# Performance work log

Hardware: AMD Instinct MI355X
Metric: run time of the kernel (lower is better)

## Reference

```python
import jax, jax.numpy as jnp
import numpy as np

N_NODES = 100000
N_EDGES = 1600000
D_FEAT = 64
EPS = 1e-07


def setup_inputs() -> dict:
    key = jax.random.key(0)
    k_x, k_r, k_c, k_b = jax.random.split(key, 4)
    x = jax.random.normal(k_x, (N_NODES, D_FEAT), dtype=jnp.float32)
    row = jax.random.randint(k_r, (N_EDGES,), 0, N_NODES, dtype=jnp.int64)
    col = jax.random.randint(k_c, (N_EDGES,), 0, N_NODES, dtype=jnp.int64)
    beta = jax.random.uniform(k_b, (), dtype=jnp.float32)  # nn.Parameter ~ U(0,1)
    return {"x": x, "row": row, "col": col, "beta": beta}


def segment_softmax(logits, seg_ids, num_segments):
    # numerically stable softmax over edges grouped by seg_ids
    seg_max = jax.ops.segment_max(logits, seg_ids, num_segments=num_segments)
    e = jnp.exp(logits - seg_max[seg_ids])
    seg_sum = jax.ops.segment_sum(e, seg_ids, num_segments=num_segments)
    return e / seg_sum[seg_ids]


def reference(x, row, col, beta):
    A = x[row]                       # [E, d] gather at source of softmax group
    B = x[col]                       # [E, d]
    inner = jnp.sum(A * B, axis=1)   # [E]
    denom = jnp.linalg.norm(A, axis=1) * jnp.linalg.norm(B, axis=1) + EPS
    sim = beta * (inner / denom)     # [E]
    P = segment_softmax(sim, row, N_NODES)          # softmax grouped by row
    src = A * P[:, None]                            # [E, d]
    out = jax.ops.segment_sum(src, col, num_segments=N_NODES)  # scatter-add by col
    return out
```

## Files before the change

### kernel.cpp

```cpp
#include <hip/hip_runtime.h>
#include <math.h>

#define N_NODES 100000
#define N_EDGES 1600000
#define D_FEAT 64
#define EPS 1e-7f
#define NPART 8
#define COLS_PER_PART (N_NODES / NPART)
#define CAP 48
#define QSCALE 12000.0f
#define QINV (1.0f / 12000.0f)

typedef _Float16 h2 __attribute__((ext_vector_type(2)));

__device__ __forceinline__ unsigned pack2h(float a, float b) {
    h2 h;
    h.x = (_Float16)a;
    h.y = (_Float16)b;
    return __builtin_bit_cast(unsigned, h);
}

__device__ __forceinline__ float dot2acc(unsigned a, unsigned b, float c) {
#if __has_builtin(__builtin_amdgcn_fdot2)
    return __builtin_amdgcn_fdot2(__builtin_bit_cast(h2, a),
                                  __builtin_bit_cast(h2, b), c, false);
#else
    h2 ha = __builtin_bit_cast(h2, a), hb = __builtin_bit_cast(h2, b);
    return c + (float)ha.x * (float)hb.x + (float)ha.y * (float)hb.y;
#endif
}

__device__ __forceinline__ void fma2h(unsigned ab, float p, float& x, float& y) {
    h2 h = __builtin_bit_cast(h2, ab);
    x += p * (float)h.x;
    y += p * (float)h.y;
}

__device__ __forceinline__ float fastrcp(float x) {
#if __has_builtin(__builtin_amdgcn_rcpf)
    return __builtin_amdgcn_rcpf(x);
#else
    return 1.0f / x;
#endif
}

__global__ void prep_kernel(const float4* __restrict__ x4, uint2* __restrict__ xh2,
                            float* __restrict__ nrm) {
    int tid = blockIdx.x * blockDim.x + threadIdx.x;
    int node = tid >> 4;
    int lane = tid & 15;
    if (node >= N_NODES) return;
    float4 v = x4[(size_t)node * 16 + lane];
    uint2 h;
    h.x = pack2h(v.x, v.y);
    h.y = pack2h(v.z, v.w);
    xh2[(size_t)node * 16 + lane] = h;
    float s = v.x * v.x + v.y * v.y + v.z * v.z + v.w * v.w;
    s += __shfl_xor(s, 1);
    s += __shfl_xor(s, 2);
    s += __shfl_xor(s, 4);
    s += __shfl_xor(s, 8);
    if (lane == 0) nrm[node] = rsqrtf(s);
}

__global__ void place_kernel(const int* __restrict__ row, const int* __restrict__ col,
                             unsigned* __restrict__ cursor, unsigned* __restrict__ pay) {
    int part = blockIdx.x & (NPART - 1);
    int blk  = blockIdx.x >> 3;
    int nblk = gridDim.x >> 3;
    int lo = part * COLS_PER_PART;
    int hi = lo + COLS_PER_PART;
    int stride = nblk * blockDim.x;
    const int4* col4 = (const int4*)col;
    for (int e4 = blk * blockDim.x + threadIdx.x; e4 < (N_EDGES >> 2); e4 += stride) {
        int4 c = col4[e4];
        int e = e4 << 2;
        if (c.x >= lo && c.x < hi) {
            unsigned pos = atomicAdd(&cursor[c.x], 1u);
            if (pos < CAP) pay[(size_t)c.x * CAP + pos] = (unsigned)row[e] << 15;
        }
        if (c.y >= lo && c.y < hi) {
            unsigned pos = atomicAdd(&cursor[c.y], 1u);
            if (pos < CAP) pay[(size_t)c.y * CAP + pos] = (unsigned)row[e + 1] << 15;
        }
        if (c.z >= lo && c.z < hi) {
            unsigned pos = atomicAdd(&cursor[c.z], 1u);
            if (pos < CAP) pay[(size_t)c.z * CAP + pos] = (unsigned)row[e + 2] << 15;
        }
        if (c.w >= lo && c.w < hi) {
            unsigned pos = atomicAdd(&cursor[c.w], 1u);
            if (pos < CAP) pay[(size_t)c.w * CAP + pos] = (unsigned)row[e + 3] << 15;
        }
    }
}

__global__ void sim_csr_kernel(const uint4* __restrict__ xh4, const float* __restrict__ nrm,
                               const unsigned* __restrict__ cursor, unsigned* __restrict__ pay,
                               const float* __restrict__ beta_p, float* __restrict__ segsum) {
    int gtid = blockIdx.x * blockDim.x + threadIdx.x;
    int node = gtid >> 6;
    if (node >= N_NODES) return;
    int lane = threadIdx.x & 63;
    int sub = lane >> 3;
    int fl  = lane & 7;
    uint4 hc = xh4[(size_t)node * 8 + fl];
    float nc = nrm[node];
    float beta = beta_p[0];
    int deg = (int)cursor[node];
    if (deg > CAP) deg = CAP;
    int start = node * CAP;
    int end = start + deg;
    for (int i0 = start; i0 < end; i0 += 32) {
        int idx = i0 + lane;
        if (idx > end - 1) idx = end - 1;
        unsigned pvL = pay[idx];
        unsigned pv0 = __shfl(pvL, sub);
        unsigned pv1 = __shfl(pvL, sub + 8);
        unsigned pv2 = __shfl(pvL, sub + 16);
        unsigned pv3 = __shfl(pvL, sub + 24);
        float nr0 = nrm[pv0 >> 15];
        float nr1 = nrm[pv1 >> 15];
        float nr2 = nrm[pv2 >> 15];
        float nr3 = nrm[pv3 >> 15];
        uint4 A0 = xh4[(size_t)(pv0 >> 15) * 8 + fl];
        uint4 A1 = xh4[(size_t)(pv1 >> 15) * 8 + fl];
        uint4 A2 = xh4[(size_t)(pv2 >> 15) * 8 + fl];
        uint4 A3 = xh4[(size_t)(pv3 >> 15) * 8 + fl];
        float d0 = 0.0f, d1 = 0.0f, d2 = 0.0f, d3 = 0.0f;
        d0 = dot2acc(A0.x, hc.x, d0); d1 = dot2acc(A1.x, hc.x, d1);
        d2 = dot2acc(A2.x, hc.x, d2); d3 = dot2acc(A3.x, hc.x, d3);
        d0 = dot2acc(A0.y, hc.y, d0); d1 = dot2acc(A1.y, hc.y, d1);
        d2 = dot2acc(A2.y, hc.y, d2); d3 = dot2acc(A3.y, hc.y, d3);
        d0 = dot2acc(A0.z, hc.z, d0); d1 = dot2acc(A1.z, hc.z, d1);
        d2 = dot2acc(A2.z, hc.z, d2); d3 = dot2acc(A3.z, hc.z, d3);
        d0 = dot2acc(A0.w, hc.w, d0); d1 = dot2acc(A1.w, hc.w, d1);
        d2 = dot2acc(A2.w, hc.w, d2); d3 = dot2acc(A3.w, hc.w, d3);
        d0 += __shfl_xor(d0, 1);  d1 += __shfl_xor(d1, 1);
        d2 += __shfl_xor(d2, 1);  d3 += __shfl_xor(d3, 1);
        d0 += __shfl_xor(d0, 2);  d1 += __shfl_xor(d1, 2);
        d2 += __shfl_xor(d2, 2);  d3 += __shfl_xor(d3, 2);
        d0 += __shfl_xor(d0, 4);  d1 += __shfl_xor(d1, 4);
        d2 += __shfl_xor(d2, 4);  d3 += __shfl_xor(d3, 4);
        float ds = d0, nrs = nr0;
        unsigned pvs = pv0;
        if (fl == 1) { ds = d1; nrs = nr1; pvs = pv1; }
        if (fl == 2) { ds = d2; nrs = nr2; pvs = pv2; }
        if (fl == 3) { ds = d3; nrs = nr3; pvs = pv3; }
        int ss = i0 + sub + (fl << 3);
        if (fl < 4 && ss < end) {
            unsigned r = pvs >> 15;
            float ex = expf(beta * (ds * nrs * nc));
            unsigned q = (unsigned)(ex * QSCALE + 0.5f);
            if (q > 32767u) q = 32767u;
            pay[ss] = pvs | q;
            atomicAdd(&segsum[r], (float)q * QINV);
        }
    }
}

__global__ void xw_kernel(uint2* __restrict__ xw2, const float* __restrict__ segsum) {
    int tid = blockIdx.x * blockDim.x + threadIdx.x;
    int node = tid >> 4;
    int lane = tid & 15;
    if (node >= N_NODES) return;
    float w = fastrcp(segsum[node]);
    uint2 h = xw2[(size_t)node * 16 + lane];
    h2 ha = __builtin_bit_cast(h2, h.x);
    h2 hb = __builtin_bit_cast(h2, h.y);
    uint2 o;
    o.x = pack2h((float)ha.x * w, (float)ha.y * w);
    o.y = pack2h((float)hb.x * w, (float)hb.y * w);
    xw2[(size_t)node * 16 + lane] = o;
}

__global__ void gather_kernel(const uint4* __restrict__ xw4, const unsigned* __restrict__ cursor,
                              const unsigned* __restrict__ pay, float4* __restrict__ out4) {
    int gtid = blockIdx.x * blockDim.x + threadIdx.x;
    int node = gtid >> 6;
    if (node >= N_NODES) return;
    int lane = threadIdx.x & 63;
    int sub = lane >> 3;
    int fl  = lane & 7;
    int deg = (int)cursor[node];
    if (deg > CAP) deg = CAP;
    int start = node * CAP;
    int end = start + deg;
    float a0 = 0.f, a1 = 0.f, a2 = 0.f, a3 = 0.f;
    float a4 = 0.f, a5 = 0.f, a6 = 0.f, a7 = 0.f;
    for (int i0 = start; i0 < end; i0 += 32) {
        int idx = i0 + lane;
        if (idx > end - 1) idx = end - 1;
        unsigned pvL = pay[idx];
        unsigned pv0 = __shfl(pvL, sub);
        unsigned pv1 = __shfl(pvL, sub + 8);
        unsigned pv2 = __shfl(pvL, sub + 16);
        unsigned pv3 = __shfl(pvL, sub + 24);
        float p0 = (i0 + sub      < end) ? (float)(pv0 & 0x7FFFu) * QINV : 0.0f;
        float p1 = (i0 + sub +  8 < end) ? (float)(pv1 & 0x7FFFu) * QINV : 0.0f;
        float p2 = (i0 + sub + 16 < end) ? (float)(pv2 & 0x7FFFu) * QINV : 0.0f;
        float p3 = (i0 + sub + 24 < end) ? (float)(pv3 & 0x7FFFu) * QINV : 0.0f;
        uint4 A0 = xw4[(size_t)(pv0 >> 15) * 8 + fl];
        uint4 A1 = xw4[(size_t)(pv1 >> 15) * 8 + fl];
        uint4 A2 = xw4[(size_t)(pv2 >> 15) * 8 + fl];
        uint4 A3 = xw4[(size_t)(pv3 >> 15) * 8 + fl];
        fma2h(A0.x, p0, a0, a1); fma2h(A1.x, p1, a0, a1);
        fma2h(A2.x, p2, a0, a1); fma2h(A3.x, p3, a0, a1);
        fma2h(A0.y, p0, a2, a3); fma2h(A1.y, p1, a2, a3);
        fma2h(A2.y, p2, a2, a3); fma2h(A3.y, p3, a2, a3);
        fma2h(A0.z, p0, a4, a5); fma2h(A1.z, p1, a4, a5);
        fma2h(A2.z, p2, a4, a5); fma2h(A3.z, p3, a4, a5);
        fma2h(A0.w, p0, a6, a7); fma2h(A1.w, p1, a6, a7);
        fma2h(A2.w, p2, a6, a7); fma2h(A3.w, p3, a6, a7);
    }
    #pragma unroll
    for (int m = 8; m <= 32; m <<= 1) {
        a0 += __shfl_xor(a0, m);
        a1 += __shfl_xor(a1, m);
        a2 += __shfl_xor(a2, m);
        a3 += __shfl_xor(a3, m);
        a4 += __shfl_xor(a4, m);
        a5 += __shfl_xor(a5, m);
        a6 += __shfl_xor(a6, m);
        a7 += __shfl_xor(a7, m);
    }
    if (sub == 0) {
        out4[(size_t)node * 16 + fl * 2]     = make_float4(a0, a1, a2, a3);
        out4[(size_t)node * 16 + fl * 2 + 1] = make_float4(a4, a5, a6, a7);
    }
}

extern "C" void kernel_launch(void* const* d_in, const int* in_sizes, int n_in,
                              void* d_out, int out_size, void* d_ws, size_t ws_size,
                              hipStream_t stream) {
    const float* x      = (const float*)d_in[0];
    const int*   row    = (const int*)d_in[1];
    const int*   col    = (const int*)d_in[2];
    const float* beta_p = (const float*)d_in[3];
    const float4* x4 = (const float4*)x;
    float4* out4 = (float4*)d_out;

    const size_t PAYB = (size_t)N_NODES * CAP * 4;
    const size_t XH   = (size_t)N_NODES * D_FEAT * 2;
    const size_t S    = 400064;
    char* ws = (char*)d_ws;
    unsigned* pay    = (unsigned*)ws;
    uint2*    xh2    = (uint2*)(ws + PAYB);
    const uint4* xh4 = (const uint4*)(ws + PAYB);
    const uint4* xw4 = (const uint4*)(ws + PAYB);
    char* base2 = ws + PAYB + XH;
    float*    segsum = (float*)(base2 + 0 * S);
    unsigned* cursor = (unsigned*)(base2 + 1 * S);
    float*    nrm    = (float*)(base2 + 2 * S);

    const int B = 256;

    hipMemsetAsync(base2, 0, 2 * S, stream);

    const int norm_blocks = (N_NODES * 16) / B;
    prep_kernel<<<norm_blocks, B, 0, stream>>>(x4, xh2, nrm);

    place_kernel<<<2048, B, 0, stream>>>(row, col, cursor, pay);

    int node_wave_grid = (N_NODES * 64) / B;
    sim_csr_kernel<<<node_wave_grid, B, 0, stream>>>(xh4, nrm, cursor, pay, beta_p, segsum);

    xw_kernel<<<norm_blocks, B, 0, stream>>>(xh2, segsum);

    gather_kernel<<<node_wave_grid, B, 0, stream>>>(xw4, cursor, pay, out4);
}
```

Before: 291.5 us.

## Merge prep and place kernels and fold softmax normalization into gather

The independent prep (fp16 conversion plus norms) and place (bucketing edges by column) kernels now run as one launch, with the block index choosing the role, so the two can overlap. The xw kernel that pre-scaled features by 1/segsum is removed. The gather kernel instead reads segsum for each edge's source row and multiplies the reciprocal into the edge weight. This saves one kernel launch and a full read/write pass over the fp16 feature table, at the cost of an extra random 4-byte load per edge in gather.

```diff
diff --git a/kernel.cpp b/kernel.cpp
--- a/kernel.cpp
+++ b/kernel.cpp
@@ -44,52 +44,54 @@
 #endif
 }
 
-__global__ void prep_kernel(const float4* __restrict__ x4, uint2* __restrict__ xh2,
-                            float* __restrict__ nrm) {
-    int tid = blockIdx.x * blockDim.x + threadIdx.x;
-    int node = tid >> 4;
-    int lane = tid & 15;
-    if (node >= N_NODES) return;
-    float4 v = x4[(size_t)node * 16 + lane];
-    uint2 h;
-    h.x = pack2h(v.x, v.y);
-    h.y = pack2h(v.z, v.w);
-    xh2[(size_t)node * 16 + lane] = h;
-    float s = v.x * v.x + v.y * v.y + v.z * v.z + v.w * v.w;
-    s += __shfl_xor(s, 1);
-    s += __shfl_xor(s, 2);
-    s += __shfl_xor(s, 4);
-    s += __shfl_xor(s, 8);
-    if (lane == 0) nrm[node] = rsqrtf(s);
-}
-
-__global__ void place_kernel(const int* __restrict__ row, const int* __restrict__ col,
-                             unsigned* __restrict__ cursor, unsigned* __restrict__ pay) {
-    int part = blockIdx.x & (NPART - 1);
-    int blk  = blockIdx.x >> 3;
-    int nblk = gridDim.x >> 3;
-    int lo = part * COLS_PER_PART;
-    int hi = lo + COLS_PER_PART;
-    int stride = nblk * blockDim.x;
-    const int4* col4 = (const int4*)col;
-    for (int e4 = blk * blockDim.x + threadIdx.x; e4 < (N_EDGES >> 2); e4 += stride) {
-        int4 c = col4[e4];
-        int e = e4 << 2;
-        if (c.x >= lo && c.x < hi) {
-            unsigned pos = atomicAdd(&cursor[c.x], 1u);
-            if (pos < CAP) pay[(size_t)c.x * CAP + pos] = (unsigned)row[e] << 15;
-        }
-        if (c.y >= lo && c.y < hi) {
-            unsigned pos = atomicAdd(&cursor[c.y], 1u);
-            if (pos < CAP) pay[(size_t)c.y * CAP + pos] = (unsigned)row[e + 1] << 15;
-        }
-        if (c.z >= lo && c.z < hi) {
-            unsigned pos = atomicAdd(&cursor[c.z], 1u);
-            if (pos < CAP) pay[(size_t)c.z * CAP + pos] = (unsigned)row[e + 2] << 15;
-        }
-        if (c.w >= lo && c.w < hi) {
-            unsigned pos = atomicAdd(&cursor[c.w], 1u);
-            if (pos < CAP) pay[(size_t)c.w * CAP + pos] = (unsigned)row[e + 3] << 15;
+__global__ void prep_place_kernel(const float4* __restrict__ x4, uint2* __restrict__ xh2,
+                                  float* __restrict__ nrm, const int* __restrict__ row,
+                                  const int* __restrict__ col, unsigned* __restrict__ cursor,
+                                  unsigned* __restrict__ pay, int norm_blocks) {
+    if ((int)blockIdx.x < norm_blocks) {
+        int tid = blockIdx.x * blockDim.x + threadIdx.x;
+        int node = tid >> 4;
+        int lane = tid & 15;
+        if (node >= N_NODES) return;
+        float4 v = x4[(size_t)node * 16 + lane];
+        uint2 h;
+        h.x = pack2h(v.x, v.y);
+        h.y = pack2h(v.z, v.w);
+        xh2[(size_t)node * 16 + lane] = h;
+        float s = v.x * v.x + v.y * v.y + v.z * v.z + v.w * v.w;
+        s += __shfl_xor(s, 1);
+        s += __shfl_xor(s, 2);
+        s += __shfl_xor(s, 4);
+        s += __shfl_xor(s, 8);
+        if (lane == 0) nrm[node] = rsqrtf(s);
+    } else {
+        int hb = blockIdx.x - norm_blocks;
+        int part = hb & (NPART - 1);
+        int blk  = hb >> 3;
+        int nblk = (gridDim.x - norm_blocks) >> 3;
+        int lo = part * COLS_PER_PART;
+        int hi = lo + COLS_PER_PART;
+        int stride = nblk * blockDim.x;
+        const int4* col4 = (const int4*)col;
+        for (int e4 = blk * blockDim.x + threadIdx.x; e4 < (N_EDGES >> 2); e4 += stride) {
+            int4 c = col4[e4];
+            int e = e4 << 2;
+            if (c.x >= lo && c.x < hi) {
+                unsigned pos = atomicAdd(&cursor[c.x], 1u);
+                if (pos < CAP) pay[(size_t)c.x * CAP + pos] = (unsigned)row[e] << 15;
+            }
+            if (c.y >= lo && c.y < hi) {
+                unsigned pos = atomicAdd(&cursor[c.y], 1u);
+                if (pos < CAP) pay[(size_t)c.y * CAP + pos] = (unsigned)row[e + 1] << 15;
+            }
+            if (c.z >= lo && c.z < hi) {
+                unsigned pos = atomicAdd(&cursor[c.z], 1u);
+                if (pos < CAP) pay[(size_t)c.z * CAP + pos] = (unsigned)row[e + 2] << 15;
+            }
+            if (c.w >= lo && c.w < hi) {
+                unsigned pos = atomicAdd(&cursor[c.w], 1u);
+                if (pos < CAP) pay[(size_t)c.w * CAP + pos] = (unsigned)row[e + 3] << 15;
+            }
         }
     }
 }
@@ -158,23 +160,9 @@
     }
 }
 
-__global__ void xw_kernel(uint2* __restrict__ xw2, const float* __restrict__ segsum) {
-    int tid = blockIdx.x * blockDim.x + threadIdx.x;
-    int node = tid >> 4;
-    int lane = tid & 15;
-    if (node >= N_NODES) return;
-    float w = fastrcp(segsum[node]);
-    uint2 h = xw2[(size_t)node * 16 + lane];
-    h2 ha = __builtin_bit_cast(h2, h.x);
-    h2 hb = __builtin_bit_cast(h2, h.y);
-    uint2 o;
-    o.x = pack2h((float)ha.x * w, (float)ha.y * w);
-    o.y = pack2h((float)hb.x * w, (float)hb.y * w);
-    xw2[(size_t)node * 16 + lane] = o;
-}
-
-__global__ void gather_kernel(const uint4* __restrict__ xw4, const unsigned* __restrict__ cursor,
-                              const unsigned* __restrict__ pay, float4* __restrict__ out4) {
+__global__ void gather_kernel(const uint4* __restrict__ xh4, const float* __restrict__ segsum,
+                              const unsigned* __restrict__ cursor, const unsigned* __restrict__ pay,
+                              float4* __restrict__ out4) {
     int gtid = blockIdx.x * blockDim.x + threadIdx.x;
     int node = gtid >> 6;
     if (node >= N_NODES) return;
@@ -195,14 +183,15 @@
         unsigned pv1 = __shfl(pvL, sub + 8);
         unsigned pv2 = __shfl(pvL, sub + 16);
         unsigned pv3 = __shfl(pvL, sub + 24);
-        float p0 = (i0 + sub      < end) ? (float)(pv0 & 0x7FFFu) * QINV : 0.0f;
-        float p1 = (i0 + sub +  8 < end) ? (float)(pv1 & 0x7FFFu) * QINV : 0.0f;
-        float p2 = (i0 + sub + 16 < end) ? (float)(pv2 & 0x7FFFu) * QINV : 0.0f;
-        float p3 = (i0 + sub + 24 < end) ? (float)(pv3 & 0x7FFFu) * QINV : 0.0f;
-        uint4 A0 = xw4[(size_t)(pv0 >> 15) * 8 + fl];
-        uint4 A1 = xw4[(size_t)(pv1 >> 15) * 8 + fl];
-        uint4 A2 = xw4[(size_t)(pv2 >> 15) * 8 + fl];
-        uint4 A3 = xw4[(size_t)(pv3 >> 15) * 8 + fl];
+        unsigned r0 = pv0 >> 15, r1 = pv1 >> 15, r2 = pv2 >> 15, r3 = pv3 >> 15;
+        float p0 = (i0 + sub      < end) ? (float)(pv0 & 0x7FFFu) * QINV * fastrcp(segsum[r0]) : 0.0f;
+        float p1 = (i0 + sub +  8 < end) ? (float)(pv1 & 0x7FFFu) * QINV * fastrcp(segsum[r1]) : 0.0f;
+        float p2 = (i0 + sub + 16 < end) ? (float)(pv2 & 0x7FFFu) * QINV * fastrcp(segsum[r2]) : 0.0f;
+        float p3 = (i0 + sub + 24 < end) ? (float)(pv3 & 0x7FFFu) * QINV * fastrcp(segsum[r3]) : 0.0f;
+        uint4 A0 = xh4[(size_t)r0 * 8 + fl];
+        uint4 A1 = xh4[(size_t)r1 * 8 + fl];
+        uint4 A2 = xh4[(size_t)r2 * 8 + fl];
+        uint4 A3 = xh4[(size_t)r3 * 8 + fl];
         fma2h(A0.x, p0, a0, a1); fma2h(A1.x, p1, a0, a1);
         fma2h(A2.x, p2, a0, a1); fma2h(A3.x, p3, a0, a1);
         fma2h(A0.y, p0, a2, a3); fma2h(A1.y, p1, a2, a3);
@@ -246,7 +235,6 @@
     unsigned* pay    = (unsigned*)ws;
     uint2*    xh2    = (uint2*)(ws + PAYB);
     const uint4* xh4 = (const uint4*)(ws + PAYB);
-    const uint4* xw4 = (const uint4*)(ws + PAYB);
     char* base2 = ws + PAYB + XH;
     float*    segsum = (float*)(base2 + 0 * S);
     unsigned* cursor = (unsigned*)(base2 + 1 * S);
@@ -256,15 +244,13 @@
 
     hipMemsetAsync(base2, 0, 2 * S, stream);
 
-    const int norm_blocks = (N_NODES * 16) / B;
-    prep_kernel<<<norm_blocks, B, 0, stream>>>(x4, xh2, nrm);
-
-    place_kernel<<<2048, B, 0, stream>>>(row, col, cursor, pay);
+    const int norm_blocks  = (N_NODES * 16) / B;
+    const int place_blocks = 2048;
+    prep_place_kernel<<<norm_blocks + place_blocks, B, 0, stream>>>(x4, xh2, nrm, row, col,
+                                                                    cursor, pay, norm_blocks);
 
     int node_wave_grid = (N_NODES * 64) / B;
     sim_csr_kernel<<<node_wave_grid, B, 0, stream>>>(xh4, nrm, cursor, pay, beta_p, segsum);
 
-    xw_kernel<<<norm_blocks, B, 0, stream>>>(xh2, segsum);
-
-    gather_kernel<<<node_wave_grid, B, 0, stream>>>(xw4, cursor, pay, out4);
-}
+    gather_kernel<<<node_wave_grid, B, 0, stream>>>(xh4, segsum, cursor, pay, out4);
+}
```

Result: faster. 284.9 us (-2.3%).
